# Performance work log

Measured on AMD Instinct MI355X. Metric: run time of the kernel, lower is better.

Reference implementation:

```python
import jax, jax.numpy as jnp
import numpy as np

LAMBDA_CM = 0.5
LAMBDA_DIV = 0.1
EPS = 1e-8


def _normalize(x):
    # F.normalize(dim=-1): x / max(||x||, 1e-12)
    n = jnp.linalg.norm(x, axis=-1, keepdims=True)
    return x / jnp.maximum(n, 1e-12)


def _cdist(z, c):
    # Euclidean pairwise distance [N, K], matching torch.cdist(p=2)
    d2 = (jnp.sum(z * z, axis=-1, keepdims=True)
          + jnp.sum(c * c, axis=-1)[None, :]
          - 2.0 * (z @ c.T))
    return jnp.sqrt(jnp.maximum(d2, 0.0))


def setup_inputs() -> dict:
    key = jax.random.key(0)
    ks = jax.random.split(key, 7)
    N, dim_a, dim_b, embed_dim, n_codes = 8192, 1024, 1024, 512, 4096
    a = jax.random.normal(ks[0], (N, dim_a), dtype=jnp.float32)
    b = jax.random.normal(ks[1], (N, dim_b), dtype=jnp.float32)
    # Linear params (kaiming-uniform-ish scale)
    Wa = jax.random.uniform(ks[2], (embed_dim, dim_a), jnp.float32, -1, 1) / np.sqrt(dim_a)
    ba = jnp.zeros((embed_dim,), jnp.float32)
    Wb = jax.random.uniform(ks[3], (embed_dim, dim_b), jnp.float32, -1, 1) / np.sqrt(dim_b)
    bb = jnp.zeros((embed_dim,), jnp.float32)
    # Orthogonal-init codebook [n_codes, embed_dim] (n_codes > embed_dim -> orthonormal columns)
    g = jax.random.normal(ks[4], (n_codes, embed_dim), dtype=jnp.float32)
    q, _ = jnp.linalg.qr(g)
    codebook = q[:, :embed_dim] if q.shape[1] >= embed_dim else g / np.sqrt(embed_dim)
    codebook = jnp.asarray(codebook, jnp.float32)
    return {"a": a, "b": b, "Wa": Wa, "ba": ba, "Wb": Wb, "bb": bb, "codebook": codebook}


def reference(a, b, Wa, ba, Wb, bb, codebook):
    sg = jax.lax.stop_gradient
    za = _normalize(a @ Wa.T + ba)  # [N, D]
    zb = _normalize(b @ Wb.T + bb)  # [N, D]

    da = _cdist(za, codebook)       # [N, K]
    db = _cdist(zb, codebook)       # [N, K]
    idx_a = jnp.argmin(da, axis=-1)
    idx_b = jnp.argmin(db, axis=-1)
    qa = codebook[idx_a]            # [N, D]
    qb = codebook[idx_b]

    mse = lambda x, y: jnp.mean((x - y) ** 2)
    rec = (mse(qa, sg(za)) + mse(qb, sg(zb))
           + 0.25 * (mse(za, sg(qa)) + mse(zb, sg(qb))))

    sim = (za @ zb.T) / 0.07        # [N, N]
    N = sim.shape[0]
    diag = jnp.arange(N)
    ce_ab = -jnp.mean(jax.nn.log_softmax(sim, axis=-1)[diag, diag])
    ce_ba = -jnp.mean(jax.nn.log_softmax(sim.T, axis=-1)[diag, diag])
    cm = (ce_ab + ce_ba) / 2

    avg_a = jnp.mean(jax.nn.softmax(-da * 5.0, axis=-1), axis=0)  # [K]
    avg_b = jnp.mean(jax.nn.softmax(-db * 5.0, axis=-1), axis=0)
    div = (-(avg_a * jnp.log(avg_a + EPS)).sum()
           - (avg_b * jnp.log(avg_b + EPS)).sum()) / 2

    loss = rec + LAMBDA_CM * cm - LAMBDA_DIV * div
    match = jnp.mean((idx_a == idx_b).astype(jnp.float32))
    return loss, match
```

## Files before the change

kernel.cpp:

```cpp
#include <hip/hip_runtime.h>
#include <hip/hip_bf16.h>
#include <math.h>
#include <float.h>

typedef __attribute__((ext_vector_type(8))) short s8bf;
typedef __attribute__((ext_vector_type(4))) float f32x4;

typedef const __attribute__((address_space(1))) void g_void;
typedef __attribute__((address_space(3))) void lds_void;

__device__ inline ushort f2bf(float x) {
    unsigned int u = __float_as_uint(x);
    unsigned int r = (u + 0x7FFFu + ((u >> 16) & 1u)) >> 16;
    return (ushort)r;
}
__device__ inline ushort f2bf_fast(float x) {
    return (ushort)((__float_as_uint(x) + 0x8000u) >> 16);
}
__device__ inline float2 bf2x2(unsigned int u) {
    float2 r;
    r.x = __uint_as_float(u << 16);
    r.y = __uint_as_float(u & 0xFFFF0000u);
    return r;
}

__global__ __launch_bounds__(256) void k_cvt_bf16(
    const float* __restrict__ src, ushort* __restrict__ dst, size_t n)
{
    size_t i = ((size_t)blockIdx.x * 256 + threadIdx.x) * 4;
    size_t stride = (size_t)gridDim.x * 256 * 4;
    for (; i < n; i += stride) {
        float4 v = *(const float4*)(src + i);
        ushort4 o;
        o.x = f2bf(v.x); o.y = f2bf(v.y); o.z = f2bf(v.z); o.w = f2bf(v.w);
        *(ushort4*)(dst + i) = o;
    }
}

__device__ inline void stage_issue2(const ushort* pa, const ushort* pb,
                                    size_t off64a, size_t off64b,
                                    ushort* As, ushort* Bs, int tid)
{
    const int wb = (tid >> 6) << 9;
    __builtin_amdgcn_global_load_lds((g_void*)pa,            (lds_void*)(As + wb),        16, 0, 0);
    __builtin_amdgcn_global_load_lds((g_void*)(pa + off64a), (lds_void*)(As + 2048 + wb), 16, 0, 0);
    __builtin_amdgcn_global_load_lds((g_void*)pb,            (lds_void*)(Bs + wb),        16, 0, 0);
    __builtin_amdgcn_global_load_lds((g_void*)(pb + off64b), (lds_void*)(Bs + 2048 + wb), 16, 0, 0);
}

__device__ inline const ushort* stage_ptr(const ushort* M, size_t ld, int ra, int tid)
{
    const int row  = tid >> 2;
    const int slot = tid & 3;
    const int scol = ((slot ^ ((row >> 1) & 3)) << 3);
    return M + (size_t)(ra + row) * ld + scol;
}

__device__ inline void mma_tile(const ushort* As, const ushort* Bs,
                                int wr, int wc, int lane, f32x4 acc[4][4])
{
    const int hi = lane >> 4, lo = lane & 15;
    const int soff = ((hi ^ ((lo >> 1) & 3)) << 3);
    s8bf af[4], bfr[4];
#pragma unroll
    for (int m = 0; m < 4; ++m)
        af[m] = *(const s8bf*)(As + (wr * 64 + m * 16 + lo) * 32 + soff);
#pragma unroll
    for (int n = 0; n < 4; ++n)
        bfr[n] = *(const s8bf*)(Bs + (wc * 64 + n * 16 + lo) * 32 + soff);
#pragma unroll
    for (int m = 0; m < 4; ++m)
#pragma unroll
        for (int n = 0; n < 4; ++n)
            acc[m][n] = __builtin_amdgcn_mfma_f32_16x16x32_bf16(
                af[m], bfr[n], acc[m][n], 0, 0, 0);
}

#define DBUF_DECL  __shared__ __align__(16) ushort Lds[2][8192]
#define AS(p) (&Lds[p][0])
#define BS(p) (&Lds[p][4096])

__global__ __launch_bounds__(256) void k_mfma_gemm_bias2(
    const ushort* __restrict__ Aa, const ushort* __restrict__ Wa,
    const float* __restrict__ ba, float* __restrict__ Ca,
    const ushort* __restrict__ Ab, const ushort* __restrict__ Wb,
    const float* __restrict__ bb, float* __restrict__ Cb,
    int Ncols, int Kd)
{
    DBUF_DECL;
    const int z = blockIdx.z;
    const ushort* A = z ? Ab : Aa;
    const ushort* W = z ? Wb : Wa;
    const float* bias = z ? bb : ba;
    float* C = z ? Cb : Ca;

    const int tid = threadIdx.x, lane = tid & 63, wid = tid >> 6;
    const int wr = wid >> 1, wc = wid & 1;
    const int rbase = blockIdx.x * 128, cbase = blockIdx.y * 128;
    const int hi = lane >> 4, lo = lane & 15;
    const int KS = Kd >> 5;
    const size_t o64 = (size_t)64 * Kd;

    f32x4 acc[4][4];
#pragma unroll
    for (int m = 0; m < 4; ++m)
#pragma unroll
        for (int n = 0; n < 4; ++n)
#pragma unroll
            for (int j = 0; j < 4; ++j) acc[m][n][j] = 0.f;

    const ushort* pa = stage_ptr(A, Kd, rbase, tid);
    const ushort* pb = stage_ptr(W, Kd, cbase, tid);
    stage_issue2(pa, pb, o64, o64, AS(0), BS(0), tid);
    __syncthreads();
    int phase = 0;
    for (int ks = 0; ks < KS; ++ks) {
        pa += 32; pb += 32;
        if (ks + 1 < KS)
            stage_issue2(pa, pb, o64, o64, AS(phase ^ 1), BS(phase ^ 1), tid);
        mma_tile(AS(phase), BS(phase), wr, wc, lane, acc);
        __syncthreads();
        phase ^= 1;
    }
#pragma unroll
    for (int n = 0; n < 4; ++n) {
        int col = cbase + wc * 64 + n * 16 + lo;
        float bv = bias[col];
#pragma unroll
        for (int m = 0; m < 4; ++m)
#pragma unroll
            for (int j = 0; j < 4; ++j) {
                int row = rbase + wr * 64 + m * 16 + hi * 4 + j;
                C[(size_t)row * Ncols + col] = acc[m][n][j] + bv;
            }
    }
}

__global__ __launch_bounds__(256) void k_normalize2(
    const float* __restrict__ Za, ushort* __restrict__ Zab,
    const float* __restrict__ Zb, ushort* __restrict__ Zbb, int N, int D)
{
    const float* Z = blockIdx.y ? Zb : Za;
    ushort* Zo = blockIdx.y ? Zbb : Zab;
    const int lane = threadIdx.x & 63, wid = threadIdx.x >> 6;
    const int row = blockIdx.x * 4 + wid;
    if (row >= N) return;
    const float4* p = (const float4*)(Z + (size_t)row * D);
    const int nf4 = D >> 2;
    float ss = 0.f;
    for (int f = lane; f < nf4; f += 64) {
        float4 v = p[f];
        ss += v.x * v.x + v.y * v.y + v.z * v.z + v.w * v.w;
    }
#pragma unroll
    for (int msk = 1; msk < 64; msk <<= 1) ss += __shfl_xor(ss, msk, 64);
    float sc = 1.0f / fmaxf(sqrtf(ss), 1e-12f);
    ushort4* pb = (ushort4*)(Zo + (size_t)row * D);
    for (int f = lane; f < nf4; f += 64) {
        float4 v = p[f];
        ushort4 u;
        u.x = f2bf(v.x * sc); u.y = f2bf(v.y * sc);
        u.z = f2bf(v.z * sc); u.w = f2bf(v.w * sc);
        pb[f] = u;
    }
}

__global__ __launch_bounds__(256) void k_rownorm2(
    const float* __restrict__ X, float* __restrict__ out, int N, int D)
{
    const int lane = threadIdx.x & 63, wid = threadIdx.x >> 6;
    const int row = blockIdx.x * 4 + wid;
    if (row >= N) return;
    const float4* p = (const float4*)(X + (size_t)row * D);
    const int nf4 = D >> 2;
    float ss = 0.f;
    for (int f = lane; f < nf4; f += 64) {
        float4 v = p[f];
        ss += v.x * v.x + v.y * v.y + v.z * v.z + v.w * v.w;
    }
#pragma unroll
    for (int msk = 1; msk < 64; msk <<= 1) ss += __shfl_xor(ss, msk, 64);
    if (lane == 0) out[row] = ss;
}

__global__ __launch_bounds__(256) void k_mfma_dist1_lite(
    const ushort* __restrict__ Za, const ushort* __restrict__ Zb,
    const ushort* __restrict__ CB, const float* __restrict__ cn,
    ushort* __restrict__ expm_a, ushort* __restrict__ expm_b,
    int Ntot, int Ktot, int D, int chunkCols)
{
    DBUF_DECL;
    const int z = blockIdx.z;
    const ushort* Z = z ? Zb : Za;
    ushort* expm = z ? expm_b : expm_a;
    const int tid = threadIdx.x, lane = tid & 63, wid = tid >> 6;
    const int wr = wid >> 1, wc = wid & 1;
    const int rbase = blockIdx.x * 128;
    const int c0 = blockIdx.y * chunkCols;
    const int hi = lane >> 4, lo = lane & 15;
    const int KS = D >> 5, TILES = chunkCols >> 7;
    const size_t o64 = (size_t)64 * D;
    const ptrdiff_t dWrapA = -(ptrdiff_t)(D - 32);
    const ptrdiff_t dWrapB = (ptrdiff_t)128 * D - (ptrdiff_t)(D - 32);

    const ushort* pa = stage_ptr(Z, D, rbase, tid);
    const ushort* pb = stage_ptr(CB, D, c0, tid);
    stage_issue2(pa, pb, o64, o64, AS(0), BS(0), tid);
    __syncthreads();
    int phase = 0;
    for (int t = 0; t < TILES; ++t) {
        f32x4 acc[4][4];
#pragma unroll
        for (int m = 0; m < 4; ++m)
#pragma unroll
            for (int n = 0; n < 4; ++n)
#pragma unroll
                for (int j = 0; j < 4; ++j) acc[m][n][j] = 0.f;
        for (int ks = 0; ks < KS; ++ks) {
            const bool wrap = (ks + 1 == KS);
            pa += wrap ? dWrapA : 32;
            pb += wrap ? dWrapB : 32;
            if (!(wrap && t + 1 == TILES))
                stage_issue2(pa, pb, o64, o64, AS(phase ^ 1), BS(phase ^ 1), tid);
            mma_tile(AS(phase), BS(phase), wr, wc, lane, acc);
            __syncthreads();
            phase ^= 1;
        }
        const int cbase = c0 + (t << 7) + wc * 64;
        float cnv[4];
#pragma unroll
        for (int n = 0; n < 4; ++n) cnv[n] = 1.0f + cn[cbase + n * 16 + lo];
#pragma unroll
        for (int m = 0; m < 4; ++m)
#pragma unroll
            for (int j = 0; j < 4; ++j) {
                ushort* erow = expm +
                    (size_t)(rbase + wr * 64 + m * 16 + hi * 4 + j) * Ktot + cbase + lo;
#pragma unroll
                for (int n = 0; n < 4; ++n) {
                    float d = sqrtf(fmaxf(cnv[n] - 2.0f * acc[m][n][j], 0.f));
                    erow[n * 16] = f2bf_fast(__expf(-5.0f * d));
                }
            }
    }
}

__global__ __launch_bounds__(256) void k_row_stats(
    const ushort* __restrict__ expm_a, const ushort* __restrict__ expm_b,
    int* __restrict__ idx_a, float* __restrict__ lse_a, float* __restrict__ inv_a,
    int* __restrict__ idx_b, float* __restrict__ lse_b, float* __restrict__ inv_b,
    int Ktot)
{
    const int z = blockIdx.y;
    const ushort* expm = z ? expm_b : expm_a;
    int* idx = z ? idx_b : idx_a;
    float* lse = z ? lse_b : lse_a;
    float* inv = z ? inv_b : inv_a;
    const int lane = threadIdx.x & 63, wid = threadIdx.x >> 6;
    const int row = blockIdx.x * 4 + wid;
    const uint4* p = (const uint4*)(expm + (size_t)row * Ktot);
    const int nf8 = Ktot >> 3;
    float s = 0.f, best = -1.f;
    int bk = 0;
    for (int f = lane; f < nf8; f += 64) {
        uint4 u = p[f];
        const unsigned* w = (const unsigned*)&u;
        const int k0 = f << 3;
#pragma unroll
        for (int q = 0; q < 4; ++q) {
            float2 e = bf2x2(w[q]);
            s += e.x + e.y;
            if (e.x > best) { best = e.x; bk = k0 + 2 * q; }
            if (e.y > best) { best = e.y; bk = k0 + 2 * q + 1; }
        }
    }
#pragma unroll
    for (int msk = 1; msk < 64; msk <<= 1) {
        float ob = __shfl_xor(best, msk, 64);
        int   ok = __shfl_xor(bk, msk, 64);
        s += __shfl_xor(s, msk, 64);
        if (ob > best || (ob == best && ok < bk)) { best = ob; bk = ok; }
    }
    if (lane == 0) {
        idx[row] = bk;
        lse[row] = __logf(s);
        inv[row] = 1.0f / s;
    }
}

__global__ __launch_bounds__(256) void k_avg_stream(
    const ushort* __restrict__ expm_a, const ushort* __restrict__ expm_b,
    const float* __restrict__ inv_a, const float* __restrict__ inv_b,
    float* __restrict__ avg_a, float* __restrict__ avg_b,
    int Ktot, int rows)
{
    const int z = blockIdx.z;
    const ushort* expm = z ? expm_b : expm_a;
    const float* invL = z ? inv_b : inv_a;
    float* avg = z ? avg_b : avg_a;
    const int c = blockIdx.x * 1024 + threadIdx.x * 4;
    const int r0 = blockIdx.y * rows;
    float4 s = {0.f, 0.f, 0.f, 0.f};
    for (int r = r0; r < r0 + rows; ++r) {
        float il = invL[r];
        uint2 u = *(const uint2*)(expm + (size_t)r * Ktot + c);
        float2 e0 = bf2x2(u.x);
        float2 e1 = bf2x2(u.y);
        s.x = fmaf(e0.x, il, s.x);
        s.y = fmaf(e0.y, il, s.y);
        s.z = fmaf(e1.x, il, s.z);
        s.w = fmaf(e1.y, il, s.w);
    }
    atomicAdd(&avg[c + 0], s.x);
    atomicAdd(&avg[c + 1], s.y);
    atomicAdd(&avg[c + 2], s.z);
    atomicAdd(&avg[c + 3], s.w);
}

__global__ __launch_bounds__(256) void k_mfma_dist1_noexp(
    const ushort* __restrict__ Za, const ushort* __restrict__ Zb,
    const ushort* __restrict__ CB,
    const float* __restrict__ cn, float* __restrict__ pd,
    float* __restrict__ pls, int* __restrict__ pib,
    int Ntot, int D, int chunkCols)
{
    DBUF_DECL;
    const int z = blockIdx.z;
    const ushort* Z = z ? Zb : Za;
    const int tid = threadIdx.x, lane = tid & 63, wid = tid >> 6;
    const int wr = wid >> 1, wc = wid & 1;
    const int rbase = blockIdx.x * 128;
    const int c0 = blockIdx.y * chunkCols;
    const int hi = lane >> 4, lo = lane & 15;
    const int KS = D >> 5, TILES = chunkCols >> 7;
    const size_t o64 = (size_t)64 * D;
    const ptrdiff_t dWrapA = -(ptrdiff_t)(D - 32);
    const ptrdiff_t dWrapB = (ptrdiff_t)128 * D - (ptrdiff_t)(D - 32);

    float bd[16], ls[16]; int bi[16];
#pragma unroll
    for (int i = 0; i < 16; ++i) { bd[i] = FLT_MAX; ls[i] = 0.f; bi[i] = 0; }

    const ushort* pa = stage_ptr(Z, D, rbase, tid);
    const ushort* pb = stage_ptr(CB, D, c0, tid);
    stage_issue2(pa, pb, o64, o64, AS(0), BS(0), tid);
    __syncthreads();
    int phase = 0;
    for (int t = 0; t < TILES; ++t) {
        f32x4 acc[4][4];
#pragma unroll
        for (int m = 0; m < 4; ++m)
#pragma unroll
            for (int n = 0; n < 4; ++n)
#pragma unroll
                for (int j = 0; j < 4; ++j) acc[m][n][j] = 0.f;
        for (int ks = 0; ks < KS; ++ks) {
            const bool wrap = (ks + 1 == KS);
            pa += wrap ? dWrapA : 32;
            pb += wrap ? dWrapB : 32;
            if (!(wrap && t + 1 == TILES))
                stage_issue2(pa, pb, o64, o64, AS(phase ^ 1), BS(phase ^ 1), tid);
            mma_tile(AS(phase), BS(phase), wr, wc, lane, acc);
            __syncthreads();
            phase ^= 1;
        }
        const int cbase = c0 + (t << 7) + wc * 64;
        float cnv[4]; int cix[4];
#pragma unroll
        for (int n = 0; n < 4; ++n) {
            cix[n] = cbase + n * 16 + lo;
            cnv[n] = cn[cix[n]];
        }
#pragma unroll
        for (int m = 0; m < 4; ++m)
#pragma unroll
            for (int j = 0; j < 4; ++j) {
                const int i = m * 4 + j;
#pragma unroll
                for (int n = 0; n < 4; ++n) {
                    float d = sqrtf(fmaxf(1.0f + cnv[n] - 2.0f * acc[m][n][j], 0.f));
                    if (d < bd[i]) { bd[i] = d; bi[i] = cix[n]; }
                    ls[i] += __expf(-5.0f * d);
                }
            }
    }
#pragma unroll
    for (int i = 0; i < 16; ++i) {
#pragma unroll
        for (int msk = 1; msk < 16; msk <<= 1) {
            float od = __shfl_xor(bd[i], msk, 64);
            int   oi = __shfl_xor(bi[i], msk, 64);
            ls[i] += __shfl_xor(ls[i], msk, 64);
            if (od < bd[i] || (od == bd[i] && oi < bi[i])) { bd[i] = od; bi[i] = oi; }
        }
    }
    if (lo == 0) {
        const int slot = (z * gridDim.y + blockIdx.y) * 2 + wc;
#pragma unroll
        for (int m = 0; m < 4; ++m)
#pragma unroll
            for (int j = 0; j < 4; ++j) {
                int row = rbase + wr * 64 + m * 16 + hi * 4 + j;
                pd [(size_t)slot * Ntot + row] = bd[m * 4 + j];
                pls[(size_t)slot * Ntot + row] = ls[m * 4 + j];
                pib[(size_t)slot * Ntot + row] = bi[m * 4 + j];
            }
    }
}

__global__ __launch_bounds__(256) void k_dist1_reduce2(
    const float* __restrict__ pd, const float* __restrict__ pls,
    const int* __restrict__ pib,
    int* __restrict__ idx_a, float* __restrict__ lse_a, float* __restrict__ inv_a,
    int* __restrict__ idx_b, float* __restrict__ lse_b, float* __restrict__ inv_b,
    int Ntot, int slots)
{
    const int z = blockIdx.y;
    int row = blockIdx.x * 256 + threadIdx.x;
    if (row >= Ntot) return;
    const float* pdz = pd + (size_t)z * slots * Ntot;
    const float* plz = pls + (size_t)z * slots * Ntot;
    const int*   piz = pib + (size_t)z * slots * Ntot;
    float bd = FLT_MAX; int bi = 0;
    float L = 0.f;
    for (int s = 0; s < slots; ++s) {
        float d = pdz[(size_t)s * Ntot + row];
        int   i = piz[(size_t)s * Ntot + row];
        if (d < bd || (d == bd && i < bi)) { bd = d; bi = i; }
        L += plz[(size_t)s * Ntot + row];
    }
    if (z) { idx_b[row] = bi; lse_b[row] = __logf(L); inv_b[row] = 1.0f / L; }
    else   { idx_a[row] = bi; lse_a[row] = __logf(L); inv_a[row] = 1.0f / L; }
}

__global__ __launch_bounds__(256) void k_mfma_dist2(
    const ushort* __restrict__ Za, const ushort* __restrict__ Zb,
    const ushort* __restrict__ CB, const float* __restrict__ cn,
    const float* __restrict__ lse_a, const float* __restrict__ lse_b,
    float* __restrict__ avg_a, float* __restrict__ avg_b,
    int Ntot, int D, int chunkCols)
{
    DBUF_DECL;
    const ushort* Z = blockIdx.z ? Zb : Za;
    const float* lse = blockIdx.z ? lse_b : lse_a;
    float* avg = blockIdx.z ? avg_b : avg_a;
    const int tid = threadIdx.x, lane = tid & 63, wid = tid >> 6;
    const int wr = wid >> 1, wc = wid & 1;
    const int rbase = blockIdx.x * 128;
    const int c0 = blockIdx.y * chunkCols;
    const int hi = lane >> 4, lo = lane & 15;
    const int KS = D >> 5, TILES = chunkCols >> 7;
    const size_t o64 = (size_t)64 * D;
    const ptrdiff_t dWrapA = -(ptrdiff_t)(D - 32);
    const ptrdiff_t dWrapB = (ptrdiff_t)128 * D - (ptrdiff_t)(D - 32);

    float lr[16];
#pragma unroll
    for (int m = 0; m < 4; ++m)
#pragma unroll
        for (int j = 0; j < 4; ++j)
            lr[m * 4 + j] = lse[rbase + wr * 64 + m * 16 + hi * 4 + j];

    const ushort* pa = stage_ptr(Z, D, rbase, tid);
    const ushort* pb = stage_ptr(CB, D, c0, tid);
    stage_issue2(pa, pb, o64, o64, AS(0), BS(0), tid);
    __syncthreads();
    int phase = 0;
    for (int t = 0; t < TILES; ++t) {
        f32x4 acc[4][4];
#pragma unroll
        for (int m = 0; m < 4; ++m)
#pragma unroll
            for (int n = 0; n < 4; ++n)
#pragma unroll
                for (int j = 0; j < 4; ++j) acc[m][n][j] = 0.f;
        for (int ks = 0; ks < KS; ++ks) {
            const bool wrap = (ks + 1 == KS);
            pa += wrap ? dWrapA : 32;
            pb += wrap ? dWrapB : 32;
            if (!(wrap && t + 1 == TILES))
                stage_issue2(pa, pb, o64, o64, AS(phase ^ 1), BS(phase ^ 1), tid);
            mma_tile(AS(phase), BS(phase), wr, wc, lane, acc);
            __syncthreads();
            phase ^= 1;
        }
        const int cbase = c0 + (t << 7) + wc * 64;
        float cnv[4];
#pragma unroll
        for (int n = 0; n < 4; ++n) cnv[n] = cn[cbase + n * 16 + lo];
        float colsum[4] = {0.f, 0.f, 0.f, 0.f};
#pragma unroll
        for (int m = 0; m < 4; ++m)
#pragma unroll
            for (int j = 0; j < 4; ++j) {
                const int i = m * 4 + j;
#pragma unroll
                for (int n = 0; n < 4; ++n) {
                    float d = sqrtf(fmaxf(1.0f + cnv[n] - 2.0f * acc[m][n][j], 0.f));
                    colsum[n] += __expf(-5.0f * d - lr[i]);
                }
            }
#pragma unroll
        for (int n = 0; n < 4; ++n) {
            float cs = colsum[n];
            cs += __shfl_xor(cs, 16, 64);
            cs += __shfl_xor(cs, 32, 64);
            if (hi == 0) atomicAdd(&avg[cbase + n * 16 + lo], cs);
        }
    }
}

__global__ __launch_bounds__(256) void k_mfma_sim_bilse(
    const ushort* __restrict__ X, const ushort* __restrict__ Y,
    float* __restrict__ pl, float* __restrict__ colsum,
    int Ntot, int D, int chunkCols)
{
    DBUF_DECL;
    const int tid = threadIdx.x, lane = tid & 63, wid = tid >> 6;
    const int wr = wid >> 1, wc = wid & 1;
    const int rbase = blockIdx.x * 128;
    const int c0 = blockIdx.y * chunkCols;
    const int hi = lane >> 4, lo = lane & 15;
    const float inv_t = 1.0f / 0.07f;
    const int KS = D >> 5, TILES = chunkCols >> 7;
    const size_t o64 = (size_t)64 * D;
    const ptrdiff_t dWrapA = -(ptrdiff_t)(D - 32);
    const ptrdiff_t dWrapB = (ptrdiff_t)128 * D - (ptrdiff_t)(D - 32);

    float Ls[16];
#pragma unroll
    for (int i = 0; i < 16; ++i) Ls[i] = 0.f;

    const ushort* pa = stage_ptr(X, D, rbase, tid);
    const ushort* pb = stage_ptr(Y, D, c0, tid);
    stage_issue2(pa, pb, o64, o64, AS(0), BS(0), tid);
    __syncthreads();
    int phase = 0;
    for (int t = 0; t < TILES; ++t) {
        f32x4 acc[4][4];
#pragma unroll
        for (int m = 0; m < 4; ++m)
#pragma unroll
            for (int n = 0; n < 4; ++n)
#pragma unroll
                for (int j = 0; j < 4; ++j) acc[m][n][j] = 0.f;
        for (int ks = 0; ks < KS; ++ks) {
            const bool wrap = (ks + 1 == KS);
            pa += wrap ? dWrapA : 32;
            pb += wrap ? dWrapB : 32;
            if (!(wrap && t + 1 == TILES))
                stage_issue2(pa, pb, o64, o64, AS(phase ^ 1), BS(phase ^ 1), tid);
            mma_tile(AS(phase), BS(phase), wr, wc, lane, acc);
            __syncthreads();
            phase ^= 1;
        }
        float csum[4] = {0.f, 0.f, 0.f, 0.f};
#pragma unroll
        for (int m = 0; m < 4; ++m)
#pragma unroll
            for (int j = 0; j < 4; ++j) {
                const int i = m * 4 + j;
#pragma unroll
                for (int n = 0; n < 4; ++n) {
                    float e = __expf(acc[m][n][j] * inv_t);
                    Ls[i] += e;
                    csum[n] += e;
                }
            }
        const int cbase = c0 + (t << 7) + wc * 64;
#pragma unroll
        for (int n = 0; n < 4; ++n) {
            float cs = csum[n];
            cs += __shfl_xor(cs, 16, 64);
            cs += __shfl_xor(cs, 32, 64);
            if (hi == 0) atomicAdd(&colsum[cbase + n * 16 + lo], cs);
        }
    }
#pragma unroll
    for (int i = 0; i < 16; ++i) {
#pragma unroll
        for (int msk = 1; msk < 16; msk <<= 1)
            Ls[i] += __shfl_xor(Ls[i], msk, 64);
    }
    if (lo == 0) {
        const int slot = blockIdx.y * 2 + wc;
#pragma unroll
        for (int m = 0; m < 4; ++m)
#pragma unroll
            for (int j = 0; j < 4; ++j) {
                int row = rbase + wr * 64 + m * 16 + hi * 4 + j;
                pl[(size_t)slot * Ntot + row] = Ls[m * 4 + j];
            }
    }
}

__global__ __launch_bounds__(256) void k_sum_log_reduce(
    const float* __restrict__ pl, float* __restrict__ out, int Ntot, int slots)
{
    int row = blockIdx.x * 256 + threadIdx.x;
    if (row >= Ntot) return;
    float L = 0.f;
    for (int s = 0; s < slots; ++s)
        L += pl[(size_t)s * Ntot + row];
    out[row] = __logf(L);
}

__global__ __launch_bounds__(256) void k_log_inplace(
    const float* __restrict__ src, float* __restrict__ dst, int n)
{
    int i = blockIdx.x * 256 + threadIdx.x;
    if (i < n) dst[i] = __logf(src[i]);
}

__global__ __launch_bounds__(256) void k_rec_match(
    const ushort* __restrict__ za, const ushort* __restrict__ zb,
    const ushort* __restrict__ cbk,
    const int* __restrict__ idx_a, const int* __restrict__ idx_b,
    const float* __restrict__ lse_ab, const float* __restrict__ lse_ba,
    float* __restrict__ acc, int N, int D)
{
    const int tid = threadIdx.x, lane = tid & 63, wid = tid >> 6;
    const int gw = blockIdx.x * 4 + wid;
    const int nw = gridDim.x * 4;
    const int nf8 = D >> 3;
    float pa = 0.f, pb = 0.f, pdot = 0.f;
    for (int row = gw; row < N; row += nw) {
        const int ia = idx_a[row], ib = idx_b[row];
        const uint4* pza = (const uint4*)(za + (size_t)row * D);
        const uint4* pzb = (const uint4*)(zb + (size_t)row * D);
        const uint4* pca = (const uint4*)(cbk + (size_t)ia * D);
        const uint4* pcb = (const uint4*)(cbk + (size_t)ib * D);
        for (int f = lane; f < nf8; f += 64) {
            uint4 ua = pza[f], ub = pzb[f], uc = pca[f], ud = pcb[f];
            const unsigned int* wa = (const unsigned int*)&ua;
            const unsigned int* wb = (const unsigned int*)&ub;
            const unsigned int* wc2 = (const unsigned int*)&uc;
            const unsigned int* wd = (const unsigned int*)&ud;
#pragma unroll
            for (int q = 0; q < 4; ++q) {
                float2 va = bf2x2(wa[q]), vb = bf2x2(wb[q]);
                float2 ca = bf2x2(wc2[q]), cb = bf2x2(wd[q]);
                float dx = va.x - ca.x, dy = va.y - ca.y;
                pa += dx * dx + dy * dy;
                dx = vb.x - cb.x; dy = vb.y - cb.y;
                pb += dx * dx + dy * dy;
                pdot += va.x * vb.x + va.y * vb.y;
            }
        }
    }
    float slab = 0.f, slba = 0.f, smatch = 0.f;
    for (int r = blockIdx.x * 256 + tid; r < N; r += gridDim.x * 256) {
        slab += lse_ab[r];
        slba += lse_ba[r];
        if (idx_a[r] == idx_b[r]) smatch += 1.f;
    }
#pragma unroll
    for (int msk = 1; msk < 64; msk <<= 1) {
        pa += __shfl_xor(pa, msk, 64);
        pb += __shfl_xor(pb, msk, 64);
        pdot += __shfl_xor(pdot, msk, 64);
        slab += __shfl_xor(slab, msk, 64);
        slba += __shfl_xor(slba, msk, 64);
        smatch += __shfl_xor(smatch, msk, 64);
    }
    __shared__ float red[4][6];
    if (lane == 0) {
        red[wid][0] = pa; red[wid][1] = pb; red[wid][2] = slab;
        red[wid][3] = slba; red[wid][4] = smatch; red[wid][5] = pdot;
    }
    __syncthreads();
    if (tid < 6) {
        float s = red[0][tid] + red[1][tid] + red[2][tid] + red[3][tid];
        atomicAdd(&acc[tid], s);
    }
}

__global__ __launch_bounds__(256) void k_finalize(
    const float* __restrict__ avg_a, const float* __restrict__ avg_b,
    const float* __restrict__ acc, float* __restrict__ out,
    int N, int D, int K)
{
    __shared__ float red[256];
    const int tid = threadIdx.x;
    const float invN = 1.0f / (float)N;
    float sa = 0.f, sb = 0.f;
    for (int k = tid; k < K; k += 256) {
        float va = avg_a[k] * invN;
        float vb = avg_b[k] * invN;
        sa += va * logf(va + 1e-8f);
        sb += vb * logf(vb + 1e-8f);
    }
    red[tid] = sa;
    __syncthreads();
    for (int s = 128; s > 0; s >>= 1) {
        if (tid < s) red[tid] += red[tid + s];
        __syncthreads();
    }
    float entA = -red[0];
    __syncthreads();
    red[tid] = sb;
    __syncthreads();
    for (int s = 128; s > 0; s >>= 1) {
        if (tid < s) red[tid] += red[tid + s];
        __syncthreads();
    }
    if (tid == 0) {
        float entB = -red[0];
        float nd = (float)N * (float)D;
        float rec = 1.25f * (acc[0] / nd + acc[1] / nd);
        float sdot = acc[5] / 0.07f;
        float cm  = 0.5f * ((acc[2] - sdot) + (acc[3] - sdot)) * invN;
        float div = 0.5f * (entA + entB);
        out[0] = rec + 0.5f * cm - 0.1f * div;
        out[1] = acc[4] * invN;
    }
}

extern "C" void kernel_launch(void* const* d_in, const int* in_sizes, int n_in,
                              void* d_out, int out_size, void* d_ws, size_t ws_size,
                              hipStream_t stream)
{
    const float* a   = (const float*)d_in[0];
    const float* b   = (const float*)d_in[1];
    const float* Wa  = (const float*)d_in[2];
    const float* ba  = (const float*)d_in[3];
    const float* Wb  = (const float*)d_in[4];
    const float* bb  = (const float*)d_in[5];
    const float* cbk = (const float*)d_in[6];

    const int D  = in_sizes[3];
    const int dA = in_sizes[2] / D;
    const int dB = in_sizes[4] / D;
    const int N  = in_sizes[0] / dA;
    const int K  = in_sizes[6] / D;

    char* w = (char*)d_ws;
    size_t off = 0;
    auto alloc = [&](size_t bytes) -> void* {
        void* p = w + off;
        off = (off + bytes + 255) & ~(size_t)255;
        return p;
    };
    float*  za     = (float*)alloc((size_t)N * D * 4);
    float*  zb     = (float*)alloc((size_t)N * D * 4);
    float*  cn     = (float*)alloc((size_t)K * 4);
    int*    idx_a  = (int*)  alloc((size_t)N * 4);
    int*    idx_b  = (int*)  alloc((size_t)N * 4);
    float*  lse_a  = (float*)alloc((size_t)N * 4);
    float*  lse_b  = (float*)alloc((size_t)N * 4);
    float*  inv_a  = (float*)alloc((size_t)N * 4);
    float*  inv_b  = (float*)alloc((size_t)N * 4);
    float*  lse_ab = (float*)alloc((size_t)N * 4);
    float*  lse_ba = (float*)alloc((size_t)N * 4);
    float*  avgreg = (float*)alloc(((size_t)2 * K + 8) * 4);
    float*  avg_a  = avgreg;
    float*  avg_b  = avgreg + K;
    float*  accb   = avgreg + 2 * K;
    ushort* Wa_bf  = (ushort*)alloc((size_t)D * dA * 2);
    ushort* Wb_bf  = (ushort*)alloc((size_t)D * dB * 2);
    ushort* cbk_bf = (ushort*)alloc((size_t)K * D * 2);
    ushort* regionA = (ushort*)alloc((size_t)N * dA * 2);
    ushort* a_bf  = regionA;
    ushort* za_bf = regionA;
    ushort* zb_bf = regionA + (size_t)N * D;
    ushort* regionB = (ushort*)alloc((size_t)N * dB * 2);
    ushort* b_bf   = regionB;
    float* pl     = (float*)regionB;
    float* pd     = pl  + (size_t)32 * N;
    float* pls    = pd  + (size_t)64 * N;
    int*   pib    = (int*)(pls + (size_t)64 * N);
    float* colsum = (float*)(pib + (size_t)64 * N);
    if (off > ws_size) return;
    ushort* expm_a = (ushort*)alloc((size_t)N * K * 2);
    ushort* expm_b = (ushort*)alloc((size_t)N * K * 2);
    const bool useExp = (off <= ws_size);

    dim3 blk(256);

    k_cvt_bf16<<<1024, blk, 0, stream>>>(a,   a_bf,   (size_t)N * dA);
    k_cvt_bf16<<<1024, blk, 0, stream>>>(b,   b_bf,   (size_t)N * dB);
    k_cvt_bf16<<<256,  blk, 0, stream>>>(Wa,  Wa_bf,  (size_t)D * dA);
    k_cvt_bf16<<<256,  blk, 0, stream>>>(Wb,  Wb_bf,  (size_t)D * dB);
    k_cvt_bf16<<<512,  blk, 0, stream>>>(cbk, cbk_bf, (size_t)K * D);

    k_mfma_gemm_bias2<<<dim3(N / 128, D / 128, 2), blk, 0, stream>>>(
        a_bf, Wa_bf, ba, za, b_bf, Wb_bf, bb, zb, D, dA);

    k_normalize2<<<dim3((N + 3) / 4, 2), blk, 0, stream>>>(za, za_bf, zb, zb_bf, N, D);
    k_rownorm2<<<dim3((K + 3) / 4), blk, 0, stream>>>(cbk, cn, K, D);
    hipMemsetAsync(avgreg, 0, ((size_t)2 * K + 8) * 4, stream);
    hipMemsetAsync(colsum, 0, (size_t)N * 4, stream);

    if (useExp) {
        const int dchunk = 512, dcy = K / dchunk;
        k_mfma_dist1_lite<<<dim3(N / 128, dcy, 2), blk, 0, stream>>>(
            za_bf, zb_bf, cbk_bf, cn, expm_a, expm_b, N, K, D, dchunk);
        k_row_stats<<<dim3(N / 4, 2), blk, 0, stream>>>(
            expm_a, expm_b, idx_a, lse_a, inv_a, idx_b, lse_b, inv_b, K);
        k_avg_stream<<<dim3(K / 1024, N / 64, 2), blk, 0, stream>>>(
            expm_a, expm_b, inv_a, inv_b, avg_a, avg_b, K, 64);
    } else {
        const int dchunk = 256, dcy = K / dchunk;
        dim3 dgrid(N / 128, dcy, 2);
        k_mfma_dist1_noexp<<<dgrid, blk, 0, stream>>>(
            za_bf, zb_bf, cbk_bf, cn, pd, pls, pib, N, D, dchunk);
        k_dist1_reduce2<<<dim3(N / 256, 2), blk, 0, stream>>>(
            pd, pls, pib, idx_a, lse_a, inv_a, idx_b, lse_b, inv_b, N, 2 * dcy);
        k_mfma_dist2<<<dgrid, blk, 0, stream>>>(
            za_bf, zb_bf, cbk_bf, cn, lse_a, lse_b, avg_a, avg_b, N, D, dchunk);
    }

    const int schunk = 512, scy = N / schunk;
    k_mfma_sim_bilse<<<dim3(N / 128, scy), blk, 0, stream>>>(za_bf, zb_bf, pl, colsum, N, D, schunk);
    k_sum_log_reduce<<<N / 256, blk, 0, stream>>>(pl, lse_ab, N, 2 * scy);
    k_log_inplace<<<N / 256, blk, 0, stream>>>(colsum, lse_ba, N);

    k_rec_match<<<256, blk, 0, stream>>>(za_bf, zb_bf, cbk_bf, idx_a, idx_b, lse_ab, lse_ba, accb, N, D);
    k_finalize<<<1, blk, 0, stream>>>(avg_a, avg_b, accb, (float*)d_out, N, D, K);
}
```

Before: 391.7 us.

## Replace dist and sim GEMMs with 256x256-tile, 8-wave, triple-buffered MFMA kernels

The distance and similarity MFMA kernels are rewritten to use 512-thread blocks with 8 waves and 256x256 output tiles. The K-slices are triple-buffered in LDS through async global-to-LDS loads, with explicit vmcnt waits, split barriers and setprio around the MFMA bursts. The aim is more operand reuse per tile, deeper load/compute overlap and fewer blocks and partial-LSE slots. In exchange each block uses 96KB of LDS and holds larger accumulator and Ls register arrays, which risks register pressure and lower occupancy.

Result: faster. 346.4 us (-11.5%).

```diff
diff --git a/kernel.cpp b/kernel.cpp
--- a/kernel.cpp
+++ b/kernel.cpp
@@ -37,6 +37,14 @@
     }
 }
 
+__device__ inline const ushort* stage_ptr(const ushort* M, size_t ld, int ra, int tid)
+{
+    const int row  = tid >> 2;
+    const int slot = tid & 3;
+    const int scol = ((slot ^ ((row >> 1) & 3)) << 3);
+    return M + (size_t)(ra + row) * ld + scol;
+}
+
 __device__ inline void stage_issue2(const ushort* pa, const ushort* pb,
                                     size_t off64a, size_t off64b,
                                     ushort* As, ushort* Bs, int tid)
@@ -46,14 +54,6 @@
     __builtin_amdgcn_global_load_lds((g_void*)(pa + off64a), (lds_void*)(As + 2048 + wb), 16, 0, 0);
     __builtin_amdgcn_global_load_lds((g_void*)pb,            (lds_void*)(Bs + wb),        16, 0, 0);
     __builtin_amdgcn_global_load_lds((g_void*)(pb + off64b), (lds_void*)(Bs + 2048 + wb), 16, 0, 0);
-}
-
-__device__ inline const ushort* stage_ptr(const ushort* M, size_t ld, int ra, int tid)
-{
-    const int row  = tid >> 2;
-    const int slot = tid & 3;
-    const int scol = ((slot ^ ((row >> 1) & 3)) << 3);
-    return M + (size_t)(ra + row) * ld + scol;
 }
 
 __device__ inline void mma_tile(const ushort* As, const ushort* Bs,
@@ -183,65 +183,239 @@
     if (lane == 0) out[row] = ss;
 }
 
-__global__ __launch_bounds__(256) void k_mfma_dist1_lite(
+#define EIGHT_PROLOG(XPTR, YPTR)                                               \
+    const int tid = threadIdx.x, lane = tid & 63, wid = tid >> 6;              \
+    const int wr = wid >> 2, wc = wid & 3;                                     \
+    const int hi = lane >> 4, lo = lane & 15;                                  \
+    const int fsw = ((hi ^ ((lo >> 1) & 3)) << 3);                             \
+    const int KT = D >> 5, KTm = KT - 1;                                       \
+    const int NIT = (chunkCols >> 8) << 5 >> 1; \
+    const size_t o128 = (size_t)128 * D;                                       \
+    const ushort* pa = stage_ptr(XPTR, D, rbase, tid);                         \
+    const ushort* pb = stage_ptr(YPTR, D, c0, tid);
+
+__device__ inline void issue8(ushort* Lbuf, const ushort* qa, const ushort* qb,
+                              size_t o128, int wid)
+{
+    ushort* A0 = Lbuf + (wid << 9);
+    ushort* B0 = Lbuf + 8192 + (wid << 9);
+    __builtin_amdgcn_global_load_lds((g_void*)qa,          (lds_void*)A0,          16, 0, 0);
+    __builtin_amdgcn_global_load_lds((g_void*)(qa + o128), (lds_void*)(A0 + 4096), 16, 0, 0);
+    __builtin_amdgcn_global_load_lds((g_void*)qb,          (lds_void*)B0,          16, 0, 0);
+    __builtin_amdgcn_global_load_lds((g_void*)(qb + o128), (lds_void*)(B0 + 4096), 16, 0, 0);
+}
+
+__global__ __launch_bounds__(512, 2) void k_sim8(
+    const ushort* __restrict__ X, const ushort* __restrict__ Y,
+    float* __restrict__ pl, float* __restrict__ colsum,
+    int Ntot, int D, int chunkCols)
+{
+    __shared__ __align__(16) ushort L3[3][16384];
+    const int rbase = blockIdx.x * 256;
+    const int c0 = blockIdx.y * chunkCols;
+    const float inv_t = 1.0f / 0.07f;
+    EIGHT_PROLOG(X, Y)
+
+    f32x4 acc[8][4];
+    float Ls[32];
+#pragma unroll
+    for (int m = 0; m < 8; ++m)
+#pragma unroll
+        for (int n = 0; n < 4; ++n)
+#pragma unroll
+            for (int j = 0; j < 4; ++j) acc[m][n][j] = 0.f;
+#pragma unroll
+    for (int i = 0; i < 32; ++i) Ls[i] = 0.f;
+
+    issue8(&L3[0][0], pa, pb, o128, wid);
+    pa += 32; pb += 32;
+    issue8(&L3[1][0], pa, pb, o128, wid);
+    if ((1 & KTm) == KTm) { pa -= (D - 32); pb += (size_t)256 * D - (D - 32); }
+    else { pa += 32; pb += 32; }
+
+    int ibuf = 0, sbuf = 2, kk = 0, tcol = 0;
+    for (int it = 0; it < NIT; ++it) {
+        const int s = it + 2;
+        if (s < NIT) {
+            issue8(&L3[sbuf][0], pa, pb, o128, wid);
+            if ((s & KTm) == KTm) { pa -= (D - 32); pb += (size_t)256 * D - (D - 32); }
+            else { pa += 32; pb += 32; }
+            if (++sbuf == 3) sbuf = 0;
+            asm volatile("s_waitcnt vmcnt(8)" ::: "memory");
+        } else if (it + 1 < NIT) {
+            asm volatile("s_waitcnt vmcnt(4)" ::: "memory");
+        } else {
+            asm volatile("s_waitcnt vmcnt(0)" ::: "memory");
+        }
+        __builtin_amdgcn_sched_barrier(0);
+        __builtin_amdgcn_s_barrier();
+
+        const ushort* Ab = &L3[ibuf][0];
+        const ushort* Bb = &L3[ibuf][8192];
+        s8bf bfr[4];
+#pragma unroll
+        for (int n = 0; n < 4; ++n)
+            bfr[n] = *(const s8bf*)(Bb + (wc * 64 + n * 16 + lo) * 32 + fsw);
+        __builtin_amdgcn_s_setprio(1);
+#pragma unroll
+        for (int m = 0; m < 4; ++m) {
+            s8bf a = *(const s8bf*)(Ab + (wr * 128 + m * 16 + lo) * 32 + fsw);
+#pragma unroll
+            for (int n = 0; n < 4; ++n)
+                acc[m][n] = __builtin_amdgcn_mfma_f32_16x16x32_bf16(a, bfr[n], acc[m][n], 0, 0, 0);
+        }
+        __builtin_amdgcn_s_setprio(0);
+        __builtin_amdgcn_s_barrier();
+        __builtin_amdgcn_s_setprio(1);
+#pragma unroll
+        for (int m = 4; m < 8; ++m) {
+            s8bf a = *(const s8bf*)(Ab + (wr * 128 + m * 16 + lo) * 32 + fsw);
+#pragma unroll
+            for (int n = 0; n < 4; ++n)
+                acc[m][n] = __builtin_amdgcn_mfma_f32_16x16x32_bf16(a, bfr[n], acc[m][n], 0, 0, 0);
+        }
+        __builtin_amdgcn_s_setprio(0);
+        __builtin_amdgcn_s_barrier();
+        if (++ibuf == 3) ibuf = 0;
+
+        if (++kk == KT) {
+            kk = 0;
+            const int cbase = c0 + tcol * 256 + wc * 64;
+            float csum[4] = {0.f, 0.f, 0.f, 0.f};
+#pragma unroll
+            for (int m = 0; m < 8; ++m)
+#pragma unroll
+                for (int j = 0; j < 4; ++j) {
+                    const int i = m * 4 + j;
+#pragma unroll
+                    for (int n = 0; n < 4; ++n) {
+                        float e = __expf(acc[m][n][j] * inv_t);
+                        Ls[i] += e;
+                        csum[n] += e;
+                        acc[m][n][j] = 0.f;
+                    }
+                }
+#pragma unroll
+            for (int n = 0; n < 4; ++n) {
+                float cs = csum[n];
+                cs += __shfl_xor(cs, 16, 64);
+                cs += __shfl_xor(cs, 32, 64);
+                if (hi == 0) atomicAdd(&colsum[cbase + n * 16 + lo], cs);
+            }
+            ++tcol;
+        }
+    }
+#pragma unroll
+    for (int i = 0; i < 32; ++i) {
+#pragma unroll
+        for (int msk = 1; msk < 16; msk <<= 1)
+            Ls[i] += __shfl_xor(Ls[i], msk, 64);
+    }
+    if (lo == 0) {
+        const int slot = blockIdx.y * 4 + wc;
+#pragma unroll
+        for (int m = 0; m < 8; ++m)
+#pragma unroll
+            for (int j = 0; j < 4; ++j) {
+                int row = rbase + wr * 128 + m * 16 + hi * 4 + j;
+                pl[(size_t)slot * Ntot + row] = Ls[m * 4 + j];
+            }
+    }
+}
+
+__global__ __launch_bounds__(512, 2) void k_dist8(
     const ushort* __restrict__ Za, const ushort* __restrict__ Zb,
     const ushort* __restrict__ CB, const float* __restrict__ cn,
     ushort* __restrict__ expm_a, ushort* __restrict__ expm_b,
     int Ntot, int Ktot, int D, int chunkCols)
 {
-    DBUF_DECL;
-    const int z = blockIdx.z;
-    const ushort* Z = z ? Zb : Za;
-    ushort* expm = z ? expm_b : expm_a;
-    const int tid = threadIdx.x, lane = tid & 63, wid = tid >> 6;
-    const int wr = wid >> 1, wc = wid & 1;
-    const int rbase = blockIdx.x * 128;
+    __shared__ __align__(16) ushort L3[3][16384];
+    const ushort* Z = blockIdx.z ? Zb : Za;
+    ushort* expm = blockIdx.z ? expm_b : expm_a;
+    const int rbase = blockIdx.x * 256;
     const int c0 = blockIdx.y * chunkCols;
-    const int hi = lane >> 4, lo = lane & 15;
-    const int KS = D >> 5, TILES = chunkCols >> 7;
-    const size_t o64 = (size_t)64 * D;
-    const ptrdiff_t dWrapA = -(ptrdiff_t)(D - 32);
-    const ptrdiff_t dWrapB = (ptrdiff_t)128 * D - (ptrdiff_t)(D - 32);
-
-    const ushort* pa = stage_ptr(Z, D, rbase, tid);
-    const ushort* pb = stage_ptr(CB, D, c0, tid);
-    stage_issue2(pa, pb, o64, o64, AS(0), BS(0), tid);
-    __syncthreads();
-    int phase = 0;
-    for (int t = 0; t < TILES; ++t) {
-        f32x4 acc[4][4];
-#pragma unroll
-        for (int m = 0; m < 4; ++m)
+    EIGHT_PROLOG(Z, CB)
+
+    f32x4 acc[8][4];
+#pragma unroll
+    for (int m = 0; m < 8; ++m)
+#pragma unroll
+        for (int n = 0; n < 4; ++n)
+#pragma unroll
+            for (int j = 0; j < 4; ++j) acc[m][n][j] = 0.f;
+
+    issue8(&L3[0][0], pa, pb, o128, wid);
+    pa += 32; pb += 32;
+    issue8(&L3[1][0], pa, pb, o128, wid);
+    if ((1 & KTm) == KTm) { pa -= (D - 32); pb += (size_t)256 * D - (D - 32); }
+    else { pa += 32; pb += 32; }
+
+    int ibuf = 0, sbuf = 2, kk = 0, tcol = 0;
+    for (int it = 0; it < NIT; ++it) {
+        const int s = it + 2;
+        if (s < NIT) {
+            issue8(&L3[sbuf][0], pa, pb, o128, wid);
+            if ((s & KTm) == KTm) { pa -= (D - 32); pb += (size_t)256 * D - (D - 32); }
+            else { pa += 32; pb += 32; }
+            if (++sbuf == 3) sbuf = 0;
+            asm volatile("s_waitcnt vmcnt(8)" ::: "memory");
+        } else if (it + 1 < NIT) {
+            asm volatile("s_waitcnt vmcnt(4)" ::: "memory");
+        } else {
+            asm volatile("s_waitcnt vmcnt(0)" ::: "memory");
+        }
+        __builtin_amdgcn_sched_barrier(0);
+        __builtin_amdgcn_s_barrier();
+
+        const ushort* Ab = &L3[ibuf][0];
+        const ushort* Bb = &L3[ibuf][8192];
+        s8bf bfr[4];
+#pragma unroll
+        for (int n = 0; n < 4; ++n)
+            bfr[n] = *(const s8bf*)(Bb + (wc * 64 + n * 16 + lo) * 32 + fsw);
+        __builtin_amdgcn_s_setprio(1);
+#pragma unroll
+        for (int m = 0; m < 4; ++m) {
+            s8bf a = *(const s8bf*)(Ab + (wr * 128 + m * 16 + lo) * 32 + fsw);
 #pragma unroll
             for (int n = 0; n < 4; ++n)
-#pragma unroll
-                for (int j = 0; j < 4; ++j) acc[m][n][j] = 0.f;
-        for (int ks = 0; ks < KS; ++ks) {
-            const bool wrap = (ks + 1 == KS);
-            pa += wrap ? dWrapA : 32;
-            pb += wrap ? dWrapB : 32;
-            if (!(wrap && t + 1 == TILES))
-                stage_issue2(pa, pb, o64, o64, AS(phase ^ 1), BS(phase ^ 1), tid);
-            mma_tile(AS(phase), BS(phase), wr, wc, lane, acc);
-            __syncthreads();
-            phase ^= 1;
-        }
-        const int cbase = c0 + (t << 7) + wc * 64;
-        float cnv[4];
-#pragma unroll
-        for (int n = 0; n < 4; ++n) cnv[n] = 1.0f + cn[cbase + n * 16 + lo];
-#pragma unroll
-        for (int m = 0; m < 4; ++m)
-#pragma unroll
-            for (int j = 0; j < 4; ++j) {
-                ushort* erow = expm +
-                    (size_t)(rbase + wr * 64 + m * 16 + hi * 4 + j) * Ktot + cbase + lo;
-#pragma unroll
-                for (int n = 0; n < 4; ++n) {
-                    float d = sqrtf(fmaxf(cnv[n] - 2.0f * acc[m][n][j], 0.f));
-                    erow[n * 16] = f2bf_fast(__expf(-5.0f * d));
+                acc[m][n] = __builtin_amdgcn_mfma_f32_16x16x32_bf16(a, bfr[n], acc[m][n], 0, 0, 0);
+        }
+        __builtin_amdgcn_s_setprio(0);
+        __builtin_amdgcn_s_barrier();
+        __builtin_amdgcn_s_setprio(1);
+#pragma unroll
+        for (int m = 4; m < 8; ++m) {
+            s8bf a = *(const s8bf*)(Ab + (wr * 128 + m * 16 + lo) * 32 + fsw);
+#pragma unroll
+            for (int n = 0; n < 4; ++n)
+                acc[m][n] = __builtin_amdgcn_mfma_f32_16x16x32_bf16(a, bfr[n], acc[m][n], 0, 0, 0);
+        }
+        __builtin_amdgcn_s_setprio(0);
+        __builtin_amdgcn_s_barrier();
+        if (++ibuf == 3) ibuf = 0;
+
+        if (++kk == KT) {
+            kk = 0;
+            const int cbase = c0 + tcol * 256 + wc * 64;
+            float cnv[4];
+#pragma unroll
+            for (int n = 0; n < 4; ++n) cnv[n] = 1.0f + cn[cbase + n * 16 + lo];
+#pragma unroll
+            for (int m = 0; m < 8; ++m)
+#pragma unroll
+                for (int j = 0; j < 4; ++j) {
+                    const int row = rbase + wr * 128 + m * 16 + hi * 4 + j;
+                    ushort* erow = expm + (size_t)row * Ktot + cbase + lo;
+#pragma unroll
+                    for (int n = 0; n < 4; ++n) {
+                        float d = sqrtf(fmaxf(cnv[n] - 2.0f * acc[m][n][j], 0.f));
+                        erow[n * 16] = f2bf_fast(__expf(-5.0f * d));
+                        acc[m][n][j] = 0.f;
+                    }
                 }
-            }
+            ++tcol;
+        }
     }
 }
 
@@ -507,90 +681,6 @@
             cs += __shfl_xor(cs, 32, 64);
             if (hi == 0) atomicAdd(&avg[cbase + n * 16 + lo], cs);
         }
-    }
-}
-
-__global__ __launch_bounds__(256) void k_mfma_sim_bilse(
-    const ushort* __restrict__ X, const ushort* __restrict__ Y,
-    float* __restrict__ pl, float* __restrict__ colsum,
-    int Ntot, int D, int chunkCols)
-{
-    DBUF_DECL;
-    const int tid = threadIdx.x, lane = tid & 63, wid = tid >> 6;
-    const int wr = wid >> 1, wc = wid & 1;
-    const int rbase = blockIdx.x * 128;
-    const int c0 = blockIdx.y * chunkCols;
-    const int hi = lane >> 4, lo = lane & 15;
-    const float inv_t = 1.0f / 0.07f;
-    const int KS = D >> 5, TILES = chunkCols >> 7;
-    const size_t o64 = (size_t)64 * D;
-    const ptrdiff_t dWrapA = -(ptrdiff_t)(D - 32);
-    const ptrdiff_t dWrapB = (ptrdiff_t)128 * D - (ptrdiff_t)(D - 32);
-
-    float Ls[16];
-#pragma unroll
-    for (int i = 0; i < 16; ++i) Ls[i] = 0.f;
-
-    const ushort* pa = stage_ptr(X, D, rbase, tid);
-    const ushort* pb = stage_ptr(Y, D, c0, tid);
-    stage_issue2(pa, pb, o64, o64, AS(0), BS(0), tid);
-    __syncthreads();
-    int phase = 0;
-    for (int t = 0; t < TILES; ++t) {
-        f32x4 acc[4][4];
-#pragma unroll
-        for (int m = 0; m < 4; ++m)
-#pragma unroll
-            for (int n = 0; n < 4; ++n)
-#pragma unroll
-                for (int j = 0; j < 4; ++j) acc[m][n][j] = 0.f;
-        for (int ks = 0; ks < KS; ++ks) {
-            const bool wrap = (ks + 1 == KS);
-            pa += wrap ? dWrapA : 32;
-            pb += wrap ? dWrapB : 32;
-            if (!(wrap && t + 1 == TILES))
-                stage_issue2(pa, pb, o64, o64, AS(phase ^ 1), BS(phase ^ 1), tid);
-            mma_tile(AS(phase), BS(phase), wr, wc, lane, acc);
-            __syncthreads();
-            phase ^= 1;
-        }
-        float csum[4] = {0.f, 0.f, 0.f, 0.f};
-#pragma unroll
-        for (int m = 0; m < 4; ++m)
-#pragma unroll
-            for (int j = 0; j < 4; ++j) {
-                const int i = m * 4 + j;
-#pragma unroll
-                for (int n = 0; n < 4; ++n) {
-                    float e = __expf(acc[m][n][j] * inv_t);
-                    Ls[i] += e;
-                    csum[n] += e;
-                }
-            }
-        const int cbase = c0 + (t << 7) + wc * 64;
-#pragma unroll
-        for (int n = 0; n < 4; ++n) {
-            float cs = csum[n];
-            cs += __shfl_xor(cs, 16, 64);
-            cs += __shfl_xor(cs, 32, 64);
-            if (hi == 0) atomicAdd(&colsum[cbase + n * 16 + lo], cs);
-        }
-    }
-#pragma unroll
-    for (int i = 0; i < 16; ++i) {
-#pragma unroll
-        for (int msk = 1; msk < 16; msk <<= 1)
-            Ls[i] += __shfl_xor(Ls[i], msk, 64);
-    }
-    if (lo == 0) {
-        const int slot = blockIdx.y * 2 + wc;
-#pragma unroll
-        for (int m = 0; m < 4; ++m)
-#pragma unroll
-            for (int j = 0; j < 4; ++j) {
-                int row = rbase + wr * 64 + m * 16 + hi * 4 + j;
-                pl[(size_t)slot * Ntot + row] = Ls[m * 4 + j];
-            }
     }
 }
 
@@ -776,6 +866,7 @@
     const bool useExp = (off <= ws_size);
 
     dim3 blk(256);
+    dim3 blk8(512);
 
     k_cvt_bf16<<<1024, blk, 0, stream>>>(a,   a_bf,   (size_t)N * dA);
     k_cvt_bf16<<<1024, blk, 0, stream>>>(b,   b_bf,   (size_t)N * dB);
@@ -792,8 +883,8 @@
     hipMemsetAsync(colsum, 0, (size_t)N * 4, stream);
 
     if (useExp) {
-        const int dchunk = 512, dcy = K / dchunk;
-        k_mfma_dist1_lite<<<dim3(N / 128, dcy, 2), blk, 0, stream>>>(
+        const int dchunk = 1024;
+        k_dist8<<<dim3(N / 256, K / dchunk, 2), blk8, 0, stream>>>(
             za_bf, zb_bf, cbk_bf, cn, expm_a, expm_b, N, K, D, dchunk);
         k_row_stats<<<dim3(N / 4, 2), blk, 0, stream>>>(
             expm_a, expm_b, idx_a, lse_a, inv_a, idx_b, lse_b, inv_b, K);
@@ -810,9 +901,9 @@
             za_bf, zb_bf, cbk_bf, cn, lse_a, lse_b, avg_a, avg_b, N, D, dchunk);
     }
 
-    const int schunk = 512, scy = N / schunk;
-    k_mfma_sim_bilse<<<dim3(N / 128, scy), blk, 0, stream>>>(za_bf, zb_bf, pl, colsum, N, D, schunk);
-    k_sum_log_reduce<<<N / 256, blk, 0, stream>>>(pl, lse_ab, N, 2 * scy);
+    const int schunk = 1024, scy = N / schunk;
+    k_sim8<<<dim3(N / 256, scy), blk8, 0, stream>>>(za_bf, zb_bf, pl, colsum, N, D, schunk);
+    k_sum_log_reduce<<<N / 256, blk, 0, stream>>>(pl, lse_ab, N, 4 * scy);
     k_log_inplace<<<N / 256, blk, 0, stream>>>(colsum, lse_ba, N);
 
     k_rec_match<<<256, blk, 0, stream>>>(za_bf, zb_bf, cbk_bf, idx_a, idx_b, lse_ab, lse_ba, accb, N, D);
```
